# Kernel tuning notes

Hardware: AMD Instinct MI355X
Metric: run time of the kernel (lower is better)

The kernel has to match this reference:

```python
import jax, jax.numpy as jnp
import numpy as np

V, L, H, D, S, B = 32000, 6, 16, 1024, 512, 4
DK = D // H
DF = 4 * D
EPS = 1e-5


def setup_inputs() -> dict:
    key = jax.random.key(0)
    ks = jax.random.split(key, 24)
    std = 0.02
    def w(k, shape):
        return jax.random.normal(k, shape, dtype=jnp.float32) * std
    inp = {
        'x': jax.random.randint(ks[0], (B, S), 0, V),
        'tok_emb': w(ks[1], (V, D)),
        # per-layer params stacked on leading L axis; Linear stored as [in,out]
        'wq': w(ks[2], (L, D, D)), 'bq': jnp.zeros((L, D)),
        'wk': w(ks[3], (L, D, D)), 'bk': jnp.zeros((L, D)),
        'wv': w(ks[4], (L, D, D)), 'bv': jnp.zeros((L, D)),
        'wo': w(ks[5], (L, D, D)), 'bo': jnp.zeros((L, D)),
        'ln1_g': jnp.ones((L, D)), 'ln1_b': jnp.zeros((L, D)),
        'w1': w(ks[6], (L, D, DF)), 'b1': jnp.zeros((L, DF)),
        'w2': w(ks[7], (L, DF, D)), 'b2': jnp.zeros((L, D)),
        'ln2_g': jnp.ones((L, D)), 'ln2_b': jnp.zeros((L, D)),
        'lnf_g': jnp.ones((D,)), 'lnf_b': jnp.zeros((D,)),
        'lm_w': w(ks[8], (D, V)),
    }
    return inp


def _layernorm(x, g, b):
    mu = jnp.mean(x, axis=-1, keepdims=True)
    var = jnp.mean(jnp.square(x - mu), axis=-1, keepdims=True)
    return (x - mu) * jax.lax.rsqrt(var + EPS) * g + b


def _sinusoidal_pe(seq_len, d_model):
    pos = jnp.arange(seq_len, dtype=jnp.float32)[:, None]
    div = jnp.exp(jnp.arange(0, d_model, 2, dtype=jnp.float32) * (-np.log(10000.0) / d_model))
    pe = jnp.zeros((seq_len, d_model), dtype=jnp.float32)
    pe = pe.at[:, 0::2].set(jnp.sin(pos * div))
    pe = pe.at[:, 1::2].set(jnp.cos(pos * div))
    return pe  # [S, D]


def _gpt_forward(x, tok_emb, wq, bq, wk, bk, wv, bv, wo, bo,
                 ln1_g, ln1_b, w1, b1, w2, b2, ln2_g, ln2_b,
                 lnf_g, lnf_b, lm_w):
    b, s = x.shape
    h = tok_emb[x] + _sinusoidal_pe(s, D)  # [B,S,D]
    causal = jnp.tril(jnp.ones((s, s), dtype=bool))  # True = keep
    scale = 1.0 / np.sqrt(DK)

    def block(h, p):
        (wq, bq, wk, bk, wv, bv, wo, bo,
         ln1_g, ln1_b, w1, b1, w2, b2, ln2_g, ln2_b) = p
        hn = _layernorm(h, ln1_g, ln1_b)
        q = (hn @ wq + bq).reshape(b, s, H, DK)
        k = (hn @ wk + bk).reshape(b, s, H, DK)
        v = (hn @ wv + bv).reshape(b, s, H, DK)
        scores = jnp.einsum('bqhd,bkhd->bhqk', q, k) * scale
        scores = jnp.where(causal, scores, -1e9)
        attn = jax.nn.softmax(scores, axis=-1)
        ctx = jnp.einsum('bhqk,bkhd->bqhd', attn, v).reshape(b, s, D)
        h = h + (ctx @ wo + bo)
        hn2 = _layernorm(h, ln2_g, ln2_b)
        ff = jax.nn.gelu(hn2 @ w1 + b1, approximate=False) @ w2 + b2
        return h + ff, None

    params = (wq, bq, wk, bk, wv, bv, wo, bo,
              ln1_g, ln1_b, w1, b1, w2, b2, ln2_g, ln2_b)
    h, _ = jax.lax.scan(block, h, params)
    h = _layernorm(h, lnf_g, lnf_b)
    return h @ lm_w  # [B,S,V] logits


def reference(x, tok_emb, wq, bq, wk, bk, wv, bv, wo, bo,
              ln1_g, ln1_b, w1, b1, w2, b2, ln2_g, ln2_b,
              lnf_g, lnf_b, lm_w):
    return _gpt_forward(x, tok_emb, wq, bq, wk, bk, wv, bv, wo, bo,
                        ln1_g, ln1_b, w1, b1, w2, b2, ln2_g, ln2_b,
                        lnf_g, lnf_b, lm_w)
```

## Files before the change

### kernel.cpp

```cpp
#include <hip/hip_runtime.h>
#include <hip/hip_bf16.h>
#include <math.h>

#define V_SIZE 32000
#define L_NUM 6
#define H_NUM 16
#define D_MODEL 1024
#define S_LEN 512
#define B_SZ 4
#define DF_DIM 4096
#define ROWS (B_SZ * S_LEN)
#define QKV_N (3 * D_MODEL)
#define KVBLK 64

typedef unsigned short u16;
typedef __attribute__((ext_vector_type(8))) short short8v;
typedef __attribute__((ext_vector_type(4))) float f32x4;

__device__ __forceinline__ float b2f(u16 b) {
  union { float f; unsigned u; } c; c.u = ((unsigned)b) << 16; return c.f;
}
__device__ __forceinline__ u16 f2b(float f) {
  __hip_bfloat16 h = __float2bfloat16(f);
  union { __hip_bfloat16 h; u16 u; } c; c.h = h; return c.u;
}
__device__ __forceinline__ void g2l16(const void* g, void* l) {
  __builtin_amdgcn_global_load_lds(
      (const __attribute__((address_space(1))) void*)g,
      (__attribute__((address_space(3))) void*)l, 16, 0, 0);
}

__global__ __launch_bounds__(256) void embed_kernel(
    const int* __restrict__ x, const float* __restrict__ tok_emb,
    float* __restrict__ h) {
  int row = blockIdx.x;
  int s = row % S_LEN;
  int tok = x[row];
  const float* te = tok_emb + (size_t)tok * D_MODEL;
  float* hr = h + (size_t)row * D_MODEL;
  float pos = (float)s;
  const float c = 9.210340371976184f / (float)D_MODEL;
#pragma unroll
  for (int i = 0; i < D_MODEL / 256; ++i) {
    int d = threadIdx.x + i * 256;
    float freq = expf(-(float)(d & ~1) * c);
    float ang = pos * freq;
    float pe = (d & 1) ? cosf(ang) : sinf(ang);
    hr[d] = te[d] + pe;
  }
}

__global__ __launch_bounds__(256) void layernorm_kernel(
    const float* __restrict__ in, const float* __restrict__ g,
    const float* __restrict__ b, u16* __restrict__ out) {
  const int row = blockIdx.x * 4 + (threadIdx.x >> 6);
  const int lane = threadIdx.x & 63;
  const float4* xr = (const float4*)(in + (size_t)row * D_MODEL);
  float4 v[4];
  float s1 = 0.f, s2 = 0.f;
#pragma unroll
  for (int i = 0; i < 4; ++i) {
    float4 t = xr[lane + i * 64];
    v[i] = t;
    s1 += t.x + t.y + t.z + t.w;
    s2 += t.x * t.x + t.y * t.y + t.z * t.z + t.w * t.w;
  }
#pragma unroll
  for (int off = 32; off; off >>= 1) {
    s1 += __shfl_xor(s1, off, 64);
    s2 += __shfl_xor(s2, off, 64);
  }
  const float mu = s1 * (1.0f / D_MODEL);
  const float var = s2 * (1.0f / D_MODEL) - mu * mu;
  const float rstd = rsqrtf(var + 1e-5f);
  u16* orow = out + (size_t)row * D_MODEL;
#pragma unroll
  for (int i = 0; i < 4; ++i) {
    const int d = (lane + i * 64) * 4;
    const float4 gv = *(const float4*)&g[d];
    const float4 bv = *(const float4*)&b[d];
    u16 o0 = f2b((v[i].x - mu) * rstd * gv.x + bv.x);
    u16 o1 = f2b((v[i].y - mu) * rstd * gv.y + bv.y);
    u16 o2 = f2b((v[i].z - mu) * rstd * gv.z + bv.z);
    u16 o3 = f2b((v[i].w - mu) * rstd * gv.w + bv.w);
    uint2 pk;
    pk.x = (unsigned)o0 | ((unsigned)o1 << 16);
    pk.y = (unsigned)o2 | ((unsigned)o3 << 16);
    *(uint2*)&orow[d] = pk;
  }
}

__global__ __launch_bounds__(256) void transpose_cvt(
    const float* __restrict__ W, u16* __restrict__ Wt, int K, int N,
    long out_stride) {
  __shared__ float t[64][33];
  const float* Wl = W + (size_t)blockIdx.z * K * N;
  u16* Wtl = Wt + (size_t)blockIdx.z * out_stride;
  const int n0 = blockIdx.x * 32, k0 = blockIdx.y * 64;
  const int tx = threadIdx.x & 31, ty = threadIdx.x >> 5;
#pragma unroll
  for (int i = 0; i < 64; i += 8)
    t[ty + i][tx] = Wl[(size_t)(k0 + ty + i) * N + n0 + tx];
  __syncthreads();
#pragma unroll
  for (int j = 0; j < 32; j += 8) {
    const int n = ty + j;
    u16 lo = f2b(t[2 * tx][n]);
    u16 hi = f2b(t[2 * tx + 1][n]);
    *(unsigned*)&Wtl[(size_t)(n0 + n) * K + k0 + 2 * tx] =
        (unsigned)lo | ((unsigned)hi << 16);
  }
}

__global__ __launch_bounds__(256) void pack_qkv_bias(
    const float* __restrict__ bq, const float* __restrict__ bk,
    const float* __restrict__ bv, float* __restrict__ out) {
  int i = blockIdx.x * 256 + threadIdx.x;
  int l = i / QKV_N, j = i % QKV_N;
  float v = (j < D_MODEL) ? bq[l * D_MODEL + j]
          : (j < 2 * D_MODEL) ? bk[l * D_MODEL + j - D_MODEL]
          : bv[l * D_MODEL + j - 2 * D_MODEL];
  out[i] = v;
}

template <int TM, int OUT_MODE, bool GELU_ACT, int SPLITK>
__global__ __launch_bounds__(256) void gemm_bf16(
    const u16* __restrict__ A, const u16* __restrict__ Bt,
    const float* __restrict__ bias, float* __restrict__ Cf,
    u16* __restrict__ Cb, int M, int N, int K) {
  constexpr int MF = TM / 32;
  constexpr int ALOADS = TM / 64;
  __shared__ __align__(16) u16 As[2][TM * 32];
  __shared__ __align__(16) u16 Bs[2][128 * 32];
  const int tid = threadIdx.x;
  const int wid = tid >> 6;
  const int lane = tid & 63;
  const int wr = wid >> 1, wc = wid & 1;
  const int nwg = gridDim.x;
  const int id = blockIdx.x;
  const int q = nwg >> 3, r = nwg & 7;
  const int xcd = id & 7, i0 = id >> 3;
  const int swz = (xcd < r ? xcd * (q + 1) : r * (q + 1) + (xcd - r) * q) + i0;
  const int kh = (SPLITK > 1) ? (swz & (SPLITK - 1)) : 0;
  const int rest = (SPLITK > 1) ? (swz >> 1) : swz;
  const int gm = M / TM;
  const int bm = rest % gm, bn = rest / gm;
  const int Ksub = K / SPLITK;
  const u16* Ag = A + (size_t)(bm * TM + wid * (TM / 4) + (lane >> 2)) * K +
                  (lane & 3) * 8 + kh * Ksub;
  const u16* Bg = Bt + (size_t)(bn * 128 + wid * 32 + (lane >> 2)) * K +
                  (lane & 3) * 8 + kh * Ksub;
  auto stage = [&](int buf, int k0) {
#pragma unroll
    for (int i = 0; i < ALOADS; ++i)
      g2l16(Ag + k0 + (size_t)(16 * i) * K, As[buf] + wid * (TM / 4) * 32 + 512 * i);
    g2l16(Bg + k0, Bs[buf] + wid * 1024);
    g2l16(Bg + k0 + (size_t)16 * K, Bs[buf] + wid * 1024 + 512);
  };
  f32x4 acc[MF][4] = {};
  const int fr = lane & 15;
  const int ko = (lane >> 4) * 8;
  stage(0, 0);
  __syncthreads();
  for (int k0 = 0; k0 < Ksub; k0 += 32) {
    const int cur = (k0 >> 5) & 1;
    if (k0 + 32 < Ksub) stage(cur ^ 1, k0 + 32);
    short8v a[MF], b[4];
#pragma unroll
    for (int m = 0; m < MF; ++m)
      a[m] = *(const short8v*)&As[cur][(wr * (TM / 2) + m * 16 + fr) * 32 + ko];
#pragma unroll
    for (int n = 0; n < 4; ++n)
      b[n] = *(const short8v*)&Bs[cur][(wc * 64 + n * 16 + fr) * 32 + ko];
#pragma unroll
    for (int m = 0; m < MF; ++m)
#pragma unroll
      for (int n = 0; n < 4; ++n)
        acc[m][n] = __builtin_amdgcn_mfma_f32_16x16x32_bf16(a[m], b[n], acc[m][n], 0, 0, 0);
    __syncthreads();
  }
  const int row0 = bm * TM + wr * (TM / 2) + (lane >> 4) * 4;
  const int col0 = bn * 128 + wc * 64 + fr;
#pragma unroll
  for (int m = 0; m < MF; ++m) {
#pragma unroll
    for (int n = 0; n < 4; ++n) {
      const int col = col0 + n * 16;
      float bv = (OUT_MODE == 2) ? 0.f : bias[col];
      if (SPLITK > 1 && kh != 0) bv = 0.f;
#pragma unroll
      for (int r2 = 0; r2 < 4; ++r2) {
        const int row = row0 + m * 16 + r2;
        float v = acc[m][n][r2] + bv;
        if (GELU_ACT) v = 0.5f * v * (1.0f + erff(v * 0.70710678118f));
        size_t idx = (size_t)row * N + col;
        if (OUT_MODE == 0) Cb[idx] = f2b(v);
        else if (OUT_MODE == 1) {
          if (SPLITK > 1) atomicAdd(&Cf[idx], v);
          else Cf[idx] += v;
        } else Cf[idx] = v;
      }
    }
  }
}

#define LDA_H(H)                                                            \
  _Pragma("unroll") for (int m = 0; m < 4; ++m)                             \
  _Pragma("unroll") for (int ks = 0; ks < 2; ++ks) {                        \
    const int row_ = wm * 128 + (H)*64 + m * 16 + fr;                       \
    const int g_ = (ks * 4 + hi) ^ (fr & 7);                                \
    a[m][ks] = *(const short8v*)&smem[cur * 16384 + row_ * 64 + g_ * 8];    \
  }
#define LDB_H(H)                                                            \
  _Pragma("unroll") for (int n = 0; n < 2; ++n)                             \
  _Pragma("unroll") for (int ks = 0; ks < 2; ++ks) {                        \
    const int row_ = wn * 64 + (H)*32 + n * 16 + fr;                        \
    const int g_ = (ks * 4 + hi) ^ (fr & 7);                                \
    b[n][ks] = *(const short8v*)&smem[32768 + cur * 16384 + row_ * 64 + g_ * 8]; \
  }
#define MFMA_CLUSTER(QA, QB)                                                \
  __builtin_amdgcn_s_barrier();                                             \
  asm volatile("s_waitcnt lgkmcnt(0)" ::: "memory");                        \
  __builtin_amdgcn_sched_barrier(0);                                        \
  __builtin_amdgcn_s_setprio(1);                                            \
  _Pragma("unroll") for (int ks = 0; ks < 2; ++ks)                          \
  _Pragma("unroll") for (int m = 0; m < 4; ++m)                             \
  _Pragma("unroll") for (int n = 0; n < 2; ++n)                             \
    acc[(QA)*4 + m][(QB)*2 + n] = __builtin_amdgcn_mfma_f32_16x16x32_bf16(  \
        a[m][ks], b[n][ks], acc[(QA)*4 + m][(QB)*2 + n], 0, 0, 0);          \
  __builtin_amdgcn_s_setprio(0);

__global__ __launch_bounds__(512, 2) void gemm256_lm(
    const u16* __restrict__ A, const u16* __restrict__ Bt,
    float* __restrict__ C, int M, int N, int K) {
  extern __shared__ __align__(16) u16 smem[];
  const int tid = threadIdx.x, wid = tid >> 6, lane = tid & 63;
  const int wm = wid >> 2, wn = wid & 3;
  const int fr = lane & 15, hi = lane >> 4;
  const int T = K / 64;
  const int nwg = gridDim.x, id = blockIdx.x;
  const int q = nwg >> 3, r = nwg & 7;
  const int xcd = id & 7, i0 = id >> 3;
  const int swz = (xcd < r ? xcd * (q + 1) : r * (q + 1) + (xcd - r) * q) + i0;
  const int gm = M / 256;
  const int bm = swz % gm, bn = swz / gm;
  const int rowA0 = bm * 256, rowB0 = bn * 256;
  const int rowoff = wid * 8 + (lane >> 3);
  const int gsw = ((lane & 7) ^ (lane >> 3)) * 8;
  auto stA = [&](int qq, int tt, int bb) {
    g2l16(A + (size_t)(rowA0 + qq * 64 + rowoff) * K + tt * 64 + gsw,
          smem + bb * 16384 + qq * 4096 + wid * 512);
  };
  auto stB = [&](int qq, int tt, int bb) {
    g2l16(Bt + (size_t)(rowB0 + qq * 64 + rowoff) * K + tt * 64 + gsw,
          smem + 32768 + bb * 16384 + qq * 4096 + wid * 512);
  };
  f32x4 acc[8][4] = {};
  stA(0, 0, 0); stA(2, 0, 0);
  stB(0, 0, 0); stB(1, 0, 0); stB(2, 0, 0); stB(3, 0, 0);
  stA(1, 0, 0); stA(3, 0, 0);
  if (T > 1) {
    stA(0, 1, 1); stA(2, 1, 1);
    asm volatile("s_waitcnt vmcnt(2)" ::: "memory");
  } else {
    asm volatile("s_waitcnt vmcnt(0)" ::: "memory");
  }
  __builtin_amdgcn_s_barrier();
  for (int t = 0; t < T; ++t) {
    const int cur = t & 1, nxt = cur ^ 1;
    short8v a[4][2], b[2][2];
    LDA_H(0); LDB_H(0);
    if (t + 1 < T) { stB(0, t + 1, nxt); stB(1, t + 1, nxt); }
    MFMA_CLUSTER(0, 0);
    __builtin_amdgcn_s_barrier();
    LDB_H(1);
    if (t + 1 < T) { stB(2, t + 1, nxt); stB(3, t + 1, nxt); }
    MFMA_CLUSTER(0, 1);
    __builtin_amdgcn_s_barrier();
    LDA_H(1);
    if (t + 1 < T) { stA(1, t + 1, nxt); stA(3, t + 1, nxt); }
    MFMA_CLUSTER(1, 1);
    __builtin_amdgcn_s_barrier();
    LDB_H(0);
    if (t + 2 < T) { stA(0, t + 2, cur); stA(2, t + 2, cur); }
    MFMA_CLUSTER(1, 0);
    if (t + 1 < T) {
      if (t + 2 < T) asm volatile("s_waitcnt vmcnt(2)" ::: "memory");
      else           asm volatile("s_waitcnt vmcnt(0)" ::: "memory");
      __builtin_amdgcn_s_barrier();
    }
  }
  float* lf = (float*)smem;
#pragma unroll
  for (int c = 0; c < 2; ++c) {
    __syncthreads();
    if (wm == c) {
#pragma unroll
      for (int m = 0; m < 8; ++m)
#pragma unroll
        for (int n = 0; n < 4; ++n)
#pragma unroll
          for (int rr = 0; rr < 4; ++rr)
            lf[(m * 16 + hi * 4 + rr) * 256 + wn * 64 + n * 16 + fr] =
                acc[m][n][rr];
    }
    __syncthreads();
#pragma unroll
    for (int i = 0; i < 16; ++i) {
      const int f = i * 2048 + tid * 4;
      const int rw = f >> 8, cl = f & 255;
      f32x4 v = *(const f32x4*)&lf[f];
      *(f32x4*)&C[(size_t)(rowA0 + c * 128 + rw) * N + rowB0 + cl] = v;
    }
  }
}

__global__ __launch_bounds__(256) void attn_mfma(
    const u16* __restrict__ qkv, u16* __restrict__ ctx) {
  __shared__ __align__(16) u16 smem[3 * 64 * 72];
  u16 (*Qs)[72] = (u16(*)[72])smem;
  u16 (*Ks)[72] = (u16(*)[72])(smem + 4608);
  u16 (*Vs)[72] = (u16(*)[72])(smem + 9216);
  const int qt = blockIdx.x, bh = blockIdx.y;
  const int b = bh >> 4, h = bh & 15;
  const int tid = threadIdx.x, wid = tid >> 6, lane = tid & 63;
  const int fr = lane & 15, ko = (lane >> 4) * 8;
  u16 (*Ps)[72] = (u16(*)[72])(smem + wid * 1152);
  const size_t rb = (size_t)b * S_LEN;
  const int q0 = qt * 64;
  const int hq = h * 64;
#pragma unroll
  for (int i = 0; i < 2; ++i) {
    int e = tid + i * 256, r = e >> 3, c = (e & 7) * 8;
    *(short8v*)&Qs[r][c] = *(const short8v*)&qkv[(rb + q0 + r) * QKV_N + hq + c];
  }
  __syncthreads();
  short8v qf[2];
#pragma unroll
  for (int ks = 0; ks < 2; ++ks)
    qf[ks] = *(const short8v*)&Qs[wid * 16 + fr][ks * 32 + ko];
  f32x4 acc_o[4] = {};
  float mrow[4], lrow[4];
#pragma unroll
  for (int r = 0; r < 4; ++r) { mrow[r] = -1e30f; lrow[r] = 0.f; }
  const int nt = qt + 1;
  for (int t = 0; t < nt; ++t) {
    const int k0 = t * KVBLK;
    __syncthreads();
#pragma unroll
    for (int i = 0; i < 2; ++i) {
      int e = tid + i * 256, r = e >> 3, c = (e & 7) * 8;
      *(short8v*)&Ks[r][c] =
          *(const short8v*)&qkv[(rb + k0 + r) * QKV_N + D_MODEL + hq + c];
      short8v vv = *(const short8v*)&qkv[(rb + k0 + r) * QKV_N + 2 * D_MODEL + hq + c];
#pragma unroll
      for (int j = 0; j < 8; ++j) Vs[c + j][r] = (u16)vv[j];
    }
    __syncthreads();
    f32x4 s[4] = {};
    __builtin_amdgcn_s_setprio(1);
#pragma unroll
    for (int n = 0; n < 4; ++n)
#pragma unroll
      for (int ks = 0; ks < 2; ++ks) {
        short8v kf = *(const short8v*)&Ks[n * 16 + fr][ks * 32 + ko];
        s[n] = __builtin_amdgcn_mfma_f32_16x16x32_bf16(qf[ks], kf, s[n], 0, 0, 0);
      }
    __builtin_amdgcn_s_setprio(0);
    const int rbase = q0 + wid * 16 + (lane >> 4) * 4;
#pragma unroll
    for (int r = 0; r < 4; ++r) {
      const int row_g = rbase + r;
      float vmax = -1e30f;
#pragma unroll
      for (int n = 0; n < 4; ++n) {
        float v = s[n][r] * 0.125f;
        if (k0 + n * 16 + fr > row_g) v = -1e30f;
        s[n][r] = v;
        vmax = fmaxf(vmax, v);
      }
#pragma unroll
      for (int off = 1; off < 16; off <<= 1) vmax = fmaxf(vmax, __shfl_xor(vmax, off, 64));
      const float mnew = fmaxf(mrow[r], vmax);
      const float sc = expf(mrow[r] - mnew);
      mrow[r] = mnew;
      float ssum = 0.f;
#pragma unroll
      for (int n = 0; n < 4; ++n) {
        float p = expf(s[n][r] - mnew);
        s[n][r] = p;
        ssum += p;
      }
#pragma unroll
      for (int off = 1; off < 16; off <<= 1) ssum += __shfl_xor(ssum, off, 64);
      lrow[r] = lrow[r] * sc + ssum;
#pragma unroll
      for (int n = 0; n < 4; ++n) {
        acc_o[n][r] *= sc;
        Ps[(lane >> 4) * 4 + r][n * 16 + fr] = f2b(s[n][r]);
      }
    }
    __builtin_amdgcn_s_setprio(1);
#pragma unroll
    for (int ks = 0; ks < 2; ++ks) {
      short8v pf = *(const short8v*)&Ps[fr][ks * 32 + ko];
#pragma unroll
      for (int n = 0; n < 4; ++n) {
        short8v vf = *(const short8v*)&Vs[n * 16 + fr][ks * 32 + ko];
        acc_o[n] = __builtin_amdgcn_mfma_f32_16x16x32_bf16(pf, vf, acc_o[n], 0, 0, 0);
      }
    }
    __builtin_amdgcn_s_setprio(0);
  }
#pragma unroll
  for (int r = 0; r < 4; ++r) {
    const int row_g = q0 + wid * 16 + (lane >> 4) * 4 + r;
    const float inv = 1.0f / lrow[r];
#pragma unroll
    for (int n = 0; n < 4; ++n)
      ctx[(rb + row_g) * D_MODEL + hq + n * 16 + fr] = f2b(acc_o[n][r] * inv);
  }
}

extern "C" void kernel_launch(void* const* d_in, const int* in_sizes, int n_in,
                              void* d_out, int out_size, void* d_ws, size_t ws_size,
                              hipStream_t stream) {
  const int* x = (const int*)d_in[0];
  const float* tok_emb = (const float*)d_in[1];
  const float* wq = (const float*)d_in[2];
  const float* bq = (const float*)d_in[3];
  const float* wk = (const float*)d_in[4];
  const float* bk = (const float*)d_in[5];
  const float* wv = (const float*)d_in[6];
  const float* bv = (const float*)d_in[7];
  const float* wo = (const float*)d_in[8];
  const float* bo = (const float*)d_in[9];
  const float* ln1_g = (const float*)d_in[10];
  const float* ln1_b = (const float*)d_in[11];
  const float* w1 = (const float*)d_in[12];
  const float* b1 = (const float*)d_in[13];
  const float* w2 = (const float*)d_in[14];
  const float* b2 = (const float*)d_in[15];
  const float* ln2_g = (const float*)d_in[16];
  const float* ln2_b = (const float*)d_in[17];
  const float* lnf_g = (const float*)d_in[18];
  const float* lnf_b = (const float*)d_in[19];
  const float* lm_w = (const float*)d_in[20];

  char* w = (char*)d_ws;
  float* h    = (float*)(w);
  u16*  hn    = (u16*)(w + (8ll << 20));
  u16*  qkvb  = (u16*)(w + (12ll << 20));
  u16*  cbuf  = (u16*)(w + (24ll << 20));
  u16*  ff    = qkvb;
  u16*  wqkvT = (u16*)(w + (28ll << 20));
  u16*  woT   = (u16*)(w + (64ll << 20));
  u16*  w1T   = (u16*)(w + (76ll << 20));
  u16*  w2T   = (u16*)(w + (124ll << 20));
  u16*  lmT   = (u16*)(w + (172ll << 20));
  float* bqkv = (float*)(w + (235ll << 20));

  const size_t DD = (size_t)D_MODEL * D_MODEL;
  const size_t DDF = (size_t)D_MODEL * DF_DIM;
  const long QS = (long)QKV_N * D_MODEL;
  transpose_cvt<<<dim3(32, 16, L_NUM), 256, 0, stream>>>(wq, wqkvT, D_MODEL, D_MODEL, QS);
  transpose_cvt<<<dim3(32, 16, L_NUM), 256, 0, stream>>>(wk, wqkvT + DD, D_MODEL, D_MODEL, QS);
  transpose_cvt<<<dim3(32, 16, L_NUM), 256, 0, stream>>>(wv, wqkvT + 2 * DD, D_MODEL, D_MODEL, QS);
  transpose_cvt<<<dim3(32, 16, L_NUM), 256, 0, stream>>>(wo, woT, D_MODEL, D_MODEL, (long)DD);
  transpose_cvt<<<dim3(128, 16, L_NUM), 256, 0, stream>>>(w1, w1T, D_MODEL, DF_DIM, (long)DDF);
  transpose_cvt<<<dim3(32, 64, L_NUM), 256, 0, stream>>>(w2, w2T, DF_DIM, D_MODEL, (long)DDF);
  transpose_cvt<<<dim3(V_SIZE / 32, 16, 1), 256, 0, stream>>>(lm_w, lmT, D_MODEL, V_SIZE, 0);
  pack_qkv_bias<<<L_NUM * QKV_N / 256, 256, 0, stream>>>(bq, bk, bv, bqkv);

  embed_kernel<<<ROWS, 256, 0, stream>>>(x, tok_emb, h);

  const int nQKV = (ROWS / 64) * (QKV_N / 128);
  const int nPRJ = 2 * (ROWS / 64) * (D_MODEL / 128);
  const int nFF1 = (ROWS / 64) * (DF_DIM / 128);
  const int nFF2 = 2 * (ROWS / 64) * (D_MODEL / 128);
  for (int l = 0; l < L_NUM; ++l) {
    layernorm_kernel<<<ROWS / 4, 256, 0, stream>>>(h, ln1_g + l * D_MODEL, ln1_b + l * D_MODEL, hn);
    gemm_bf16<64, 0, false, 1><<<nQKV, 256, 0, stream>>>(
        hn, wqkvT + (size_t)l * QS, bqkv + l * QKV_N, nullptr, qkvb,
        ROWS, QKV_N, D_MODEL);
    attn_mfma<<<dim3(S_LEN / 64, B_SZ * H_NUM), 256, 0, stream>>>(qkvb, cbuf);
    gemm_bf16<64, 1, false, 2><<<nPRJ, 256, 0, stream>>>(
        cbuf, woT + l * DD, bo + l * D_MODEL, h, nullptr, ROWS, D_MODEL, D_MODEL);
    layernorm_kernel<<<ROWS / 4, 256, 0, stream>>>(h, ln2_g + l * D_MODEL, ln2_b + l * D_MODEL, hn);
    gemm_bf16<64, 0, true, 1><<<nFF1, 256, 0, stream>>>(
        hn, w1T + l * DDF, b1 + l * DF_DIM, nullptr, ff, ROWS, DF_DIM, D_MODEL);
    gemm_bf16<64, 1, false, 2><<<nFF2, 256, 0, stream>>>(
        ff, w2T + l * DDF, b2 + l * D_MODEL, h, nullptr, ROWS, D_MODEL, DF_DIM);
  }
  layernorm_kernel<<<ROWS / 4, 256, 0, stream>>>(h, lnf_g, lnf_b, hn);

  hipFuncSetAttribute((const void*)gemm256_lm,
                      hipFuncAttributeMaxDynamicSharedMemorySize, 131072);
  const int nLM = (ROWS / 256) * (V_SIZE / 256);
  gemm256_lm<<<nLM, 512, 131072, stream>>>(
      hn, lmT, (float*)d_out, ROWS, V_SIZE, D_MODEL);
}
```

Measured before the change: 1.432 ms.

## Use BK=64 XOR-swizzled LDS tiles in GEMM and prefetch attention K/V into registers

The GEMM k-step grows from 32 to 64. Global-to-LDS loads are remapped to 8 rows per instruction with an XOR swizzle on 16-byte chunks, which avoids LDS bank conflicts on the fragment reads, and the MFMA block is wrapped in s_setprio. This halves the number of barrier and loop iterations per tile but doubles LDS use, which may lower occupancy. In attention, the next K/V tile is loaded into registers while the current tile is being computed, hiding global latency at the cost of more registers.

Result: no change. 1.412 ms (-1.4%).

```diff
diff --git a/kernel.cpp b/kernel.cpp
--- a/kernel.cpp
+++ b/kernel.cpp
@@ -129,9 +129,9 @@
     const float* __restrict__ bias, float* __restrict__ Cf,
     u16* __restrict__ Cb, int M, int N, int K) {
   constexpr int MF = TM / 32;
-  constexpr int ALOADS = TM / 64;
-  __shared__ __align__(16) u16 As[2][TM * 32];
-  __shared__ __align__(16) u16 Bs[2][128 * 32];
+  constexpr int AINSTS = TM / 32;
+  __shared__ __align__(16) u16 As[2][TM * 64];
+  __shared__ __align__(16) u16 Bs[2][128 * 64];
   const int tid = threadIdx.x;
   const int wid = tid >> 6;
   const int lane = tid & 63;
@@ -146,40 +146,53 @@
   const int gm = M / TM;
   const int bm = rest % gm, bn = rest / gm;
   const int Ksub = K / SPLITK;
-  const u16* Ag = A + (size_t)(bm * TM + wid * (TM / 4) + (lane >> 2)) * K +
-                  (lane & 3) * 8 + kh * Ksub;
-  const u16* Bg = Bt + (size_t)(bn * 128 + wid * 32 + (lane >> 2)) * K +
-                  (lane & 3) * 8 + kh * Ksub;
+  const int rowi = lane >> 3;
+  const int gsw = ((lane & 7) ^ rowi) * 8;
+  const u16* Ag = A + (size_t)(bm * TM + wid * (TM / 4) + rowi) * K + kh * Ksub + gsw;
+  const u16* Bg = Bt + (size_t)(bn * 128 + wid * 32 + rowi) * K + kh * Ksub + gsw;
   auto stage = [&](int buf, int k0) {
 #pragma unroll
-    for (int i = 0; i < ALOADS; ++i)
-      g2l16(Ag + k0 + (size_t)(16 * i) * K, As[buf] + wid * (TM / 4) * 32 + 512 * i);
-    g2l16(Bg + k0, Bs[buf] + wid * 1024);
-    g2l16(Bg + k0 + (size_t)16 * K, Bs[buf] + wid * 1024 + 512);
+    for (int i = 0; i < AINSTS; ++i)
+      g2l16(Ag + k0 + (size_t)(8 * i) * K, As[buf] + wid * (TM / 4) * 64 + i * 512);
+#pragma unroll
+    for (int i = 0; i < 4; ++i)
+      g2l16(Bg + k0 + (size_t)(8 * i) * K, Bs[buf] + wid * 2048 + i * 512);
   };
   f32x4 acc[MF][4] = {};
   const int fr = lane & 15;
-  const int ko = (lane >> 4) * 8;
+  const int hi = lane >> 4;
   stage(0, 0);
   __syncthreads();
-  for (int k0 = 0; k0 < Ksub; k0 += 32) {
-    const int cur = (k0 >> 5) & 1;
-    if (k0 + 32 < Ksub) stage(cur ^ 1, k0 + 32);
-    short8v a[MF], b[4];
+  for (int k0 = 0; k0 < Ksub; k0 += 64) {
+    const int cur = (k0 >> 6) & 1;
+    if (k0 + 64 < Ksub) stage(cur ^ 1, k0 + 64);
+    short8v a[MF][2], b[4][2];
 #pragma unroll
     for (int m = 0; m < MF; ++m)
-      a[m] = *(const short8v*)&As[cur][(wr * (TM / 2) + m * 16 + fr) * 32 + ko];
+#pragma unroll
+      for (int kk = 0; kk < 2; ++kk) {
+        const int g = (kk * 4 + hi) ^ (fr & 7);
+        a[m][kk] = *(const short8v*)&As[cur][(wr * (TM / 2) + m * 16 + fr) * 64 + g * 8];
+      }
 #pragma unroll
     for (int n = 0; n < 4; ++n)
-      b[n] = *(const short8v*)&Bs[cur][(wc * 64 + n * 16 + fr) * 32 + ko];
-#pragma unroll
-    for (int m = 0; m < MF; ++m)
-#pragma unroll
-      for (int n = 0; n < 4; ++n)
-        acc[m][n] = __builtin_amdgcn_mfma_f32_16x16x32_bf16(a[m], b[n], acc[m][n], 0, 0, 0);
+#pragma unroll
+      for (int kk = 0; kk < 2; ++kk) {
+        const int g = (kk * 4 + hi) ^ (fr & 7);
+        b[n][kk] = *(const short8v*)&Bs[cur][(wc * 64 + n * 16 + fr) * 64 + g * 8];
+      }
+    __builtin_amdgcn_s_setprio(1);
+#pragma unroll
+    for (int kk = 0; kk < 2; ++kk)
+#pragma unroll
+      for (int m = 0; m < MF; ++m)
+#pragma unroll
+        for (int n = 0; n < 4; ++n)
+          acc[m][n] = __builtin_amdgcn_mfma_f32_16x16x32_bf16(a[m][kk], b[n][kk], acc[m][n], 0, 0, 0);
+    __builtin_amdgcn_s_setprio(0);
     __syncthreads();
   }
-  const int row0 = bm * TM + wr * (TM / 2) + (lane >> 4) * 4;
+  const int row0 = bm * TM + wr * (TM / 2) + hi * 4;
   const int col0 = bn * 128 + wc * 64 + fr;
 #pragma unroll
   for (int m = 0; m < MF; ++m) {
@@ -344,19 +357,29 @@
 #pragma unroll
   for (int r = 0; r < 4; ++r) { mrow[r] = -1e30f; lrow[r] = 0.f; }
   const int nt = qt + 1;
+  short8v kreg[2], vreg[2];
+  auto loadregs = [&](int t) {
+    const int k0 = t * KVBLK;
+#pragma unroll
+    for (int i = 0; i < 2; ++i) {
+      const int e = tid + i * 256, rr = e >> 3, cc = (e & 7) * 8;
+      kreg[i] = *(const short8v*)&qkv[(rb + k0 + rr) * QKV_N + D_MODEL + hq + cc];
+      vreg[i] = *(const short8v*)&qkv[(rb + k0 + rr) * QKV_N + 2 * D_MODEL + hq + cc];
+    }
+  };
+  loadregs(0);
   for (int t = 0; t < nt; ++t) {
+    __syncthreads();
+#pragma unroll
+    for (int i = 0; i < 2; ++i) {
+      const int e = tid + i * 256, rr = e >> 3, cc = (e & 7) * 8;
+      *(short8v*)&Ks[rr][cc] = kreg[i];
+#pragma unroll
+      for (int j = 0; j < 8; ++j) Vs[cc + j][rr] = (u16)vreg[i][j];
+    }
+    __syncthreads();
+    if (t + 1 < nt) loadregs(t + 1);
     const int k0 = t * KVBLK;
-    __syncthreads();
-#pragma unroll
-    for (int i = 0; i < 2; ++i) {
-      int e = tid + i * 256, r = e >> 3, c = (e & 7) * 8;
-      *(short8v*)&Ks[r][c] =
-          *(const short8v*)&qkv[(rb + k0 + r) * QKV_N + D_MODEL + hq + c];
-      short8v vv = *(const short8v*)&qkv[(rb + k0 + r) * QKV_N + 2 * D_MODEL + hq + c];
-#pragma unroll
-      for (int j = 0; j < 8; ++j) Vs[c + j][r] = (u16)vv[j];
-    }
-    __syncthreads();
     f32x4 s[4] = {};
     __builtin_amdgcn_s_setprio(1);
 #pragma unroll
```
